# Kernel tuning notes

Measured on AMD Instinct MI355X. Metric: run time of the kernel, lower is better.

Reference implementation:

```python
import jax, jax.numpy as jnp
import numpy as np

D_MODEL = 1024
N_HEADS = 16
D_FF = 4 * D_MODEL
CTX = 2048
EPS = 1e-5


def setup_inputs() -> dict:
    key = jax.random.key(0)
    ks = jax.random.split(key, 8)
    s = 0.02
    z = jax.random.normal(ks[0], (2, CTX, D_MODEL), dtype=jnp.float32)
    W_Q = jax.random.normal(ks[1], (D_MODEL, D_MODEL), dtype=jnp.float32) * s
    W_K = jax.random.normal(ks[2], (D_MODEL, D_MODEL), dtype=jnp.float32) * s
    W_V = jax.random.normal(ks[3], (D_MODEL, D_MODEL), dtype=jnp.float32) * s
    W_O = jax.random.normal(ks[4], (D_MODEL, D_MODEL), dtype=jnp.float32) * s
    W_fc = jax.random.normal(ks[5], (D_MODEL, D_FF), dtype=jnp.float32) * s
    W_proj = jax.random.normal(ks[6], (D_FF, D_MODEL), dtype=jnp.float32) * s
    g1 = jnp.ones((D_MODEL,), dtype=jnp.float32)
    g2 = jnp.ones((D_MODEL,), dtype=jnp.float32)
    return {"z": z, "W_Q": W_Q, "W_K": W_K, "W_V": W_V, "W_O": W_O,
            "W_fc": W_fc, "W_proj": W_proj, "g1": g1, "g2": g2}


def rmsnorm(x, gain):
    rms = jnp.sqrt(jnp.sum(x * x, axis=-1, keepdims=True) / x.shape[-1] + EPS)
    return (x / rms) * gain


def gelu_erf(x):
    return x * 0.5 * (1.0 + jax.lax.erf(x / jnp.sqrt(2.0).astype(x.dtype)))


def attention(zn, W_Q, W_K, W_V, W_O):
    B, T, D = zn.shape
    H = N_HEADS
    dh = D // H
    # [B,T,D] -> [B,H,T,dh]
    def split(x):
        return x.reshape(B, T, H, dh).transpose(0, 2, 1, 3)
    Q = split(zn @ W_Q)
    K = split(zn @ W_K)
    V = split(zn @ W_V)
    scores = jnp.einsum('bhtd,bhsd->bhts', Q, K) / jnp.sqrt(jnp.float32(dh))
    causal = jnp.triu(jnp.ones((T, T), dtype=bool), k=1)  # True above diagonal -> masked
    scores = jnp.where(causal[None, None], -jnp.inf, scores)
    weights = jax.nn.softmax(scores, axis=-1)
    ctx = jnp.einsum('bhts,bhsd->bhtd', weights, V)
    ctx = ctx.transpose(0, 2, 1, 3).reshape(B, T, D)
    return ctx @ W_O


def reference(z, W_Q, W_K, W_V, W_O, W_fc, W_proj, g1, g2):
    # pre-norm GPT block: z + attn(norm1(z)); then + ffn(norm2(z))
    z = z + attention(rmsnorm(z, g1), W_Q, W_K, W_V, W_O)
    h = rmsnorm(z, g2)
    ffn = gelu_erf(h @ W_fc) @ W_proj
    return z + ffn
```

## Files before the change

kernel.cpp:

```cpp
#include <hip/hip_runtime.h>
#include <hip/hip_bf16.h>
#include <math.h>


typedef __bf16 bf16x8 __attribute__((ext_vector_type(8)));
typedef float  f32x4  __attribute__((ext_vector_type(4)));

#define MFMA_16x16x32_BF16(A, B, C) __builtin_amdgcn_mfma_f32_16x16x32_bf16((A), (B), (C), 0, 0, 0)

#define GLDS16(g, l) __builtin_amdgcn_global_load_lds( \
    (const __attribute__((address_space(1))) void*)(g), \
    (__attribute__((address_space(3))) void*)(l), 16, 0, 0)

__global__ __launch_bounds__(256) void fused_head_kernel(
    const float* __restrict__ W_Q, const float* __restrict__ W_K,
    const float* __restrict__ W_V, const float* __restrict__ W_O,
    const float* __restrict__ W_fc, const float* __restrict__ W_proj,
    __bf16* __restrict__ WtQKV, __bf16* __restrict__ WtO,
    __bf16* __restrict__ Wtfc, __bf16* __restrict__ Wtproj,
    const float* __restrict__ z, const float* __restrict__ g1,
    __bf16* __restrict__ zn)
{
    const int id = blockIdx.x;
    if (id >= 12288) {
        const int row = id - 12288, t = threadIdx.x;
        const float4 v = ((const float4*)(z + (size_t)row * 1024))[t];
        float ss = v.x * v.x + v.y * v.y + v.z * v.z + v.w * v.w;
#pragma unroll
        for (int m = 1; m < 64; m <<= 1) ss += __shfl_xor(ss, m);
        __shared__ float red[4];
        const int wid = t >> 6, lane = t & 63;
        if (lane == 0) red[wid] = ss;
        __syncthreads();
        const float tot = red[0] + red[1] + red[2] + red[3];
        const float inv = rsqrtf(tot * (1.0f / 1024.0f) + 1e-5f);
        const float4 gv = ((const float4*)g1)[t];
        __bf16* o = zn + (size_t)row * 1024 + t * 4;
        o[0] = (__bf16)(v.x * inv * gv.x);
        o[1] = (__bf16)(v.y * inv * gv.y);
        o[2] = (__bf16)(v.z * inv * gv.z);
        o[3] = (__bf16)(v.w * inv * gv.w);
        return;
    }
    const float* src;
    __bf16* dst;
    int K, N, nx, t;
    if (id < 4096) {
        const int wsel = id >> 10;
        t = id & 1023;
        src = (wsel == 0) ? W_Q : (wsel == 1) ? W_K : (wsel == 2) ? W_V : W_O;
        dst = (wsel < 3) ? (WtQKV + (size_t)wsel * 1048576) : WtO;
        K = 1024; N = 1024; nx = 32;
    } else if (id < 8192) {
        t = id - 4096; src = W_fc; dst = Wtfc; K = 1024; N = 4096; nx = 128;
    } else {
        t = id - 8192; src = W_proj; dst = Wtproj; K = 4096; N = 1024; nx = 32;
    }
    const int n0 = (t % nx) * 32, k0 = (t / nx) * 32;

    __shared__ float tile[32][33];
    const int c = threadIdx.x & 31, r = threadIdx.x >> 5;
#pragma unroll
    for (int i = 0; i < 4; ++i)
        tile[r + 8 * i][c] = src[(size_t)(k0 + r + 8 * i) * N + n0 + c];
    __syncthreads();
#pragma unroll
    for (int i = 0; i < 4; ++i)
        dst[(size_t)(n0 + r + 8 * i) * K + k0 + c] = (__bf16)tile[c][r + 8 * i];
}

__global__ __launch_bounds__(256) void rmsnorm_kernel(
    const float* __restrict__ x, const float* __restrict__ gain,
    __bf16* __restrict__ out)
{
    const int row = blockIdx.x, t = threadIdx.x;
    const float4 v = ((const float4*)(x + (size_t)row * 1024))[t];
    float ss = v.x * v.x + v.y * v.y + v.z * v.z + v.w * v.w;
#pragma unroll
    for (int m = 1; m < 64; m <<= 1) ss += __shfl_xor(ss, m);
    __shared__ float red[4];
    const int wid = t >> 6, lane = t & 63;
    if (lane == 0) red[wid] = ss;
    __syncthreads();
    const float tot = red[0] + red[1] + red[2] + red[3];
    const float inv = rsqrtf(tot * (1.0f / 1024.0f) + 1e-5f);
    const float4 gv = ((const float4*)gain)[t];
    __bf16* o = out + (size_t)row * 1024 + t * 4;
    o[0] = (__bf16)(v.x * inv * gv.x);
    o[1] = (__bf16)(v.y * inv * gv.y);
    o[2] = (__bf16)(v.z * inv * gv.z);
    o[3] = (__bf16)(v.w * inv * gv.w);
}

__global__ __launch_bounds__(256) void reduce_add_kernel(
    float* __restrict__ out, const float* __restrict__ p0,
    const float* __restrict__ p1, int n4)
{
    for (int i = blockIdx.x * 256 + threadIdx.x; i < n4; i += gridDim.x * 256) {
        const float4 a = ((const float4*)p0)[i];
        const float4 b = ((const float4*)p1)[i];
        float4 o = ((float4*)out)[i];
        o.x += a.x + b.x; o.y += a.y + b.y;
        o.z += a.z + b.z; o.w += a.w + b.w;
        ((float4*)out)[i] = o;
    }
}

template <int EPI>
__device__ __forceinline__ void epi_write(
    void* outp, const float* res, int N, int rowg, int colg, float v)
{
    if constexpr (EPI == 1) {
        const size_t idx = (size_t)rowg * N + colg;
        ((float*)outp)[idx] = res[idx] + v;
    } else if constexpr (EPI == 2) {
        const size_t idx = (size_t)rowg * N + colg;
        const float u = v * (1.0f + 0.044715f * v * v) * 2.3022585093f;
        const float r = __builtin_amdgcn_rcpf(1.0f + exp2f(u));
        ((__bf16*)outp)[idx] = (__bf16)(v - v * r);
    } else {
        __bf16* base = (__bf16*)outp;
        const int seg = colg >> 10;
        const int cg = colg & 1023;
        if (seg < 2) {
            base[(size_t)seg * 4194304 + (size_t)rowg * 1024 + cg] = (__bf16)v;
        } else {
            const int tt = rowg & 2047;
            const int r32 = tt & 31;
            const int p = ((r32 & 12) << 1) | ((r32 >> 2) & 4) | (r32 & 3);
            base[8388608 +
                 ((size_t)((rowg >> 11) * 16 + (cg >> 6)) * 64 + (cg & 63)) * 2048 +
                 ((tt & ~31) | p)] = (__bf16)v;
        }
    }
}

template <int EPI>
__global__ __launch_bounds__(512, 2) void gemm256(
    const __bf16* __restrict__ A, const __bf16* __restrict__ Bt,
    void* __restrict__ outp, const float* __restrict__ res,
    int M, int N, int K)
{
    __shared__ __bf16 As[2][2][128 * 64];
    __shared__ __bf16 Bs[2][2][128 * 64];
    const int tid = threadIdx.x;

    const int gx = gridDim.x, nwg = gx * gridDim.y;
    int bid = blockIdx.y * gx + blockIdx.x;
    int m0, n0;
    if (gx == 16 && gridDim.y == 16) {
        const int xcd = bid & 7, c = bid >> 3;
        const int rm = xcd >> 1, rn = xcd & 1;
        m0 = (rm * 4 + (c >> 3)) * 256;
        n0 = (rn * 8 + (c & 7)) * 256;
    } else {
        if ((nwg & 7) == 0) bid = (bid & 7) * (nwg >> 3) + (bid >> 3);
        m0 = (bid / gx) * 256; n0 = (bid % gx) * 256;
    }

    const int lane = tid & 63, w = tid >> 6;
    const int wr = w >> 2, wc = w & 3;
    const int lr = lane & 15, g = lane >> 4;
    const int srow8 = lane >> 3, schunk = (lane & 7) ^ srow8;
    const int xk = lr & 7;
    const int wch = wc >> 1, bro = (wc & 1) * 64;

    const __bf16* Ab = A + (size_t)m0 * K;
    const __bf16* Bb = Bt + (size_t)n0 * K;

    auto STG = [&](const __bf16* gb, __bf16* lds, int kt, int half) {
        const __bf16* src = gb + (size_t)(half * 128) * K + (kt << 6);
#pragma unroll
        for (int j = 0; j < 2; ++j) {
            const int sidx = j * 8 + w;
            GLDS16(src + (size_t)(sidx * 8 + srow8) * K + schunk * 8, lds + sidx * 512);
        }
    };

    f32x4 acc[8][4] = {};
    bf16x8 af[2][4], bf[2][4];

#define LAF(BUF, QM) do {                                                       \
    _Pragma("unroll") for (int i_ = 0; i_ < 4; ++i_)                            \
    _Pragma("unroll") for (int kk_ = 0; kk_ < 2; ++kk_)                         \
        af[kk_][i_] = *(const bf16x8*)&As[BUF][wr]                              \
            [((QM) * 64 + i_ * 16 + lr) * 64 + (((kk_ * 4 + g) ^ xk) << 3)];    \
    } while (0)

#define LBF(BUF, QN) do {                                                       \
    _Pragma("unroll") for (int i_ = 0; i_ < 2; ++i_)                            \
    _Pragma("unroll") for (int kk_ = 0; kk_ < 2; ++kk_)                         \
        bf[kk_][(QN) * 2 + i_] = *(const bf16x8*)&Bs[BUF][wch]                  \
            [(bro + ((QN) * 2 + i_) * 16 + lr) * 64 + (((kk_ * 4 + g) ^ xk) << 3)]; \
    } while (0)

#define MMQ(QM, QN) do {                                                        \
    __builtin_amdgcn_s_setprio(1);                                              \
    _Pragma("unroll") for (int kk_ = 0; kk_ < 2; ++kk_)                         \
    _Pragma("unroll") for (int i_ = 0; i_ < 4; ++i_)                            \
    _Pragma("unroll") for (int n_ = 0; n_ < 2; ++n_)                            \
        acc[(QM) * 4 + i_][(QN) * 2 + n_] = MFMA_16x16x32_BF16(                 \
            af[kk_][i_], bf[kk_][(QN) * 2 + n_], acc[(QM) * 4 + i_][(QN) * 2 + n_]); \
    __builtin_amdgcn_s_setprio(0);                                              \
    } while (0)

#define BAR()  __builtin_amdgcn_s_barrier()
#define VMC(N_) asm volatile("s_waitcnt vmcnt(" #N_ ")" ::: "memory")
#define SGB0() __builtin_amdgcn_sched_barrier(0)

    const int nt = K >> 6, niter = nt >> 1;

    STG(Ab, &As[0][0][0], 0, 0); STG(Ab, &As[0][1][0], 0, 1);
    STG(Bb, &Bs[0][0][0], 0, 0); STG(Bb, &Bs[0][1][0], 0, 1);
    STG(Bb, &Bs[1][0][0], 1, 0); STG(Bb, &Bs[1][1][0], 1, 1);

    for (int i = 0; i < niter - 1; ++i) {
        const int t1 = 2 * i + 1;
        STG(Ab, &As[1][0][0], t1, 0);
        VMC(6); BAR(); SGB0();
        LAF(0, 0); LBF(0, 0); MMQ(0, 0); BAR();
        LBF(0, 1); STG(Ab, &As[1][1][0], t1, 1); BAR(); MMQ(0, 1); BAR();
        LAF(0, 1); STG(Bb, &Bs[0][0][0], t1 + 1, 0); BAR(); MMQ(1, 0); BAR();
        STG(Bb, &Bs[0][1][0], t1 + 1, 1); BAR(); MMQ(1, 1); BAR();
        STG(Ab, &As[0][0][0], t1 + 1, 0);
        VMC(6); BAR(); SGB0();
        LAF(1, 0); LBF(1, 0); MMQ(0, 0); BAR();
        LBF(1, 1); STG(Ab, &As[0][1][0], t1 + 1, 1); BAR(); MMQ(0, 1); BAR();
        LAF(1, 1); STG(Bb, &Bs[1][0][0], t1 + 2, 0); BAR(); MMQ(1, 0); BAR();
        STG(Bb, &Bs[1][1][0], t1 + 2, 1); BAR(); MMQ(1, 1); BAR();
    }
    {
        STG(Ab, &As[1][0][0], nt - 1, 0);
        VMC(6); BAR(); SGB0();
        LAF(0, 0); LBF(0, 0); MMQ(0, 0); BAR();
        LBF(0, 1); STG(Ab, &As[1][1][0], nt - 1, 1); BAR(); MMQ(0, 1); BAR();
        LAF(0, 1); BAR(); MMQ(1, 0); BAR();
        BAR(); MMQ(1, 1); BAR();
        VMC(0); BAR(); SGB0();
        LAF(1, 0); LBF(1, 0); MMQ(0, 0); BAR();
        LBF(1, 1); BAR(); MMQ(0, 1); BAR();
        LAF(1, 1); BAR(); MMQ(1, 0); BAR();
        BAR(); MMQ(1, 1); BAR();
    }
#undef LAF
#undef LBF
#undef MMQ
#undef BAR
#undef VMC
#undef SGB0

#pragma unroll
    for (int mi = 0; mi < 8; ++mi)
#pragma unroll
        for (int ni = 0; ni < 4; ++ni) {
            const int colg = n0 + wc * 64 + ni * 16 + lr;
#pragma unroll
            for (int r = 0; r < 4; ++r) {
                const int rowg = m0 + wr * 128 + mi * 16 + 4 * g + r;
                epi_write<EPI>(outp, res, N, rowg, colg, acc[mi][ni][r]);
            }
        }
}

template <int BM, int BN, int EPI>
__global__ __launch_bounds__(256) void gemm_bf16(
    const __bf16* __restrict__ A, const __bf16* __restrict__ Bt,
    void* __restrict__ outp, const float* __restrict__ res,
    int M, int N, int K, int Kld)
{
    __shared__ __bf16 As[2][BM * 64];
    __shared__ __bf16 Bs[2][BN * 64];
    const int tid = threadIdx.x;

    const int gx = gridDim.x, nwg = gx * gridDim.y;
    int bid = blockIdx.y * gx + blockIdx.x;
    int m0, n0;
    if constexpr (EPI == 4) {
        const int xcd = bid & 7, c = bid >> 3;
        const int rm = xcd >> 1, rn = xcd & 1;
        m0 = (rm * 8 + c / 12) * BM;
        n0 = (rn * 12 + c % 12) * BN;
    } else {
        if ((nwg & 7) == 0) bid = (bid & 7) * (nwg >> 3) + (bid >> 3);
        m0 = (bid / gx) * BM; n0 = (bid % gx) * BN;
    }

    const int lane = tid & 63, w = tid >> 6;
    const int wm = w >> 1, wn = w & 1;
    const int lr = lane & 15, g = lane >> 4;
    const int srow = lane >> 3;
    const int scol = ((lane & 7) ^ srow) * 8;
    const int xr8 = lr & 7;

    constexpr int MI = BM / 32, NI = BN / 32;
    f32x4 acc[MI][NI] = {};

    const __bf16* Abase = A + (size_t)m0 * Kld + blockIdx.z * K;
    const __bf16* Bbase = Bt + (size_t)n0 * Kld + blockIdx.z * K;

    auto STAGE = [&](int kb, int buf) {
#pragma unroll
        for (int j = 0; j < BM / 32; ++j) {
            const int s = j * 4 + w;
            GLDS16(Abase + (size_t)(s * 8 + srow) * Kld + kb + scol, &As[buf][s * 512]);
        }
#pragma unroll
        for (int j = 0; j < BN / 32; ++j) {
            const int s = j * 4 + w;
            GLDS16(Bbase + (size_t)(s * 8 + srow) * Kld + kb + scol, &Bs[buf][s * 512]);
        }
    };

    const int nt = K >> 6;
    STAGE(0, 0);
    __syncthreads();

    for (int t = 0; t < nt; ++t) {
        const int cur = t & 1;
        if (t + 1 < nt) STAGE((t + 1) << 6, cur ^ 1);

        bf16x8 af[2][MI], bfr[2][NI];
#pragma unroll
        for (int kk = 0; kk < 2; ++kk) {
#pragma unroll
            for (int i = 0; i < MI; ++i)
                af[kk][i] = *(const bf16x8*)
                    &As[cur][(wm * (BM / 2) + i * 16 + lr) * 64 + (((kk * 4 + g) ^ xr8) << 3)];
#pragma unroll
            for (int i = 0; i < NI; ++i)
                bfr[kk][i] = *(const bf16x8*)
                    &Bs[cur][(wn * (BN / 2) + i * 16 + lr) * 64 + (((kk * 4 + g) ^ xr8) << 3)];
        }
#pragma unroll
        for (int kk = 0; kk < 2; ++kk)
#pragma unroll
            for (int mi = 0; mi < MI; ++mi)
#pragma unroll
                for (int ni = 0; ni < NI; ++ni)
                    acc[mi][ni] = MFMA_16x16x32_BF16(af[kk][mi], bfr[kk][ni], acc[mi][ni]);
        if (t + 1 < nt) __syncthreads();
    }

#pragma unroll
    for (int mi = 0; mi < MI; ++mi)
#pragma unroll
        for (int ni = 0; ni < NI; ++ni) {
            const int colg = n0 + wn * (BN / 2) + ni * 16 + lr;
#pragma unroll
            for (int r = 0; r < 4; ++r) {
                const int rowg = m0 + wm * (BM / 2) + mi * 16 + 4 * g + r;
                const float v = acc[mi][ni][r];
                if constexpr (EPI == 5) {
                    float* pout = (blockIdx.z == 0) ? (float*)outp : (float*)(void*)res;
                    pout[(size_t)rowg * N + colg] = v;
                } else {
                    epi_write<EPI>(outp, res, N, rowg, colg, v);
                }
            }
        }
}

__global__ __launch_bounds__(512) void attn_kernel(
    const __bf16* __restrict__ Q, const __bf16* __restrict__ Kb,
    const __bf16* __restrict__ Vt, __bf16* __restrict__ ctx)
{
    const int Dm = 1024, T = 2048;
    const int tid = threadIdx.x;
    const int w = tid >> 6, lane = tid & 63;
    const int lr = lane & 15, g = lane >> 4;
    const int bx = blockIdx.x;
    const int j = bx >> 5, bh = bx & 31, b = bh >> 4, h = bh & 15;
    const int qc = (j < 8) ? j : 23 - j;
    const int qbase = qc * 128 + w * 16;
    const size_t rowoff = (size_t)b * T;
    const __bf16* Qp = Q + rowoff * Dm + h * 64;
    const __bf16* Kp = Kb + rowoff * Dm + h * 64;
    const __bf16* Vtp = Vt + (size_t)bh * 64 * 2048;

    __shared__ __bf16 Ks[2][128 * 64];
    __shared__ __bf16 Vs[2][64 * 128];

    bf16x8 qf0 = *(const bf16x8*)&Qp[(size_t)(qbase + lr) * Dm + g * 8];
    bf16x8 qf1 = *(const bf16x8*)&Qp[(size_t)(qbase + lr) * Dm + 32 + g * 8];
    const float qsc = 0.125f * 1.44269504088896340736f;
#pragma unroll
    for (int jj = 0; jj < 8; ++jj) {
        qf0[jj] = (__bf16)((float)qf0[jj] * qsc);
        qf1[jj] = (__bf16)((float)qf1[jj] * qsc);
    }

    const int ksrow = lane >> 3;
    const int kschunk = (lane & 7) ^ ksrow;
    const int vsrow = lane >> 4;

    f32x4 acc[4] = {};
    float m_s = -__builtin_inff(), lpart = 0.0f;
    const int nsteps = qc + 1;
    const f32x4 zacc = {0.0f, 0.0f, 0.0f, 0.0f};
    const int x8 = lr & 7;
    const int qg = qbase + lr;

    auto STAGE = [&](int kvb, int buf) {
#pragma unroll
        for (int jj = 0; jj < 2; ++jj) {
            const int krow = w * 16 + jj * 8;
            GLDS16(Kp + (size_t)(kvb + krow + ksrow) * Dm + kschunk * 8,
                   &Ks[buf][krow * 64]);
            const int vrow = w * 8 + jj * 4;
            const int vchunk = (lane & 15) ^ ((vrow + vsrow) & 15);
            GLDS16(Vtp + (size_t)(vrow + vsrow) * T + kvb + vchunk * 8,
                   &Vs[buf][vrow * 128]);
        }
    };

    STAGE(0, 0);
    __syncthreads();

    for (int t = 0; t < nsteps; ++t) {
        const int kvb = t * 128, cur = t & 1;
        if (t + 1 < nsteps) STAGE(kvb + 128, cur ^ 1);

        float sv[8][4];
        if (t < qc) {
#pragma unroll
            for (int s4 = 0; s4 < 8; ++s4) {
                const int row = s4 * 16 + lr;
                const bf16x8 kfa = *(const bf16x8*)&Ks[cur][row * 64 + ((g ^ x8) << 3)];
                const bf16x8 kfb = *(const bf16x8*)&Ks[cur][row * 64 + (((4 + g) ^ x8) << 3)];
                f32x4 st = MFMA_16x16x32_BF16(kfa, qf0, zacc);
                st = MFMA_16x16x32_BF16(kfb, qf1, st);
#pragma unroll
                for (int r = 0; r < 4; ++r) sv[s4][r] = st[r];
            }
        } else {
#pragma unroll
            for (int s4 = 0; s4 < 8; ++s4) {
                const int kv0 = kvb + s4 * 16;
                if (kv0 <= qbase + 15) {
                    const int row = s4 * 16 + lr;
                    const bf16x8 kfa = *(const bf16x8*)&Ks[cur][row * 64 + ((g ^ x8) << 3)];
                    const bf16x8 kfb = *(const bf16x8*)&Ks[cur][row * 64 + (((4 + g) ^ x8) << 3)];
                    f32x4 st = MFMA_16x16x32_BF16(kfa, qf0, zacc);
                    st = MFMA_16x16x32_BF16(kfb, qf1, st);
                    const bool domask = (kv0 + 15 > qbase);
#pragma unroll
                    for (int r = 0; r < 4; ++r) {
                        float x = st[r];
                        if (domask && (kv0 + 4 * g + r > qg)) x = -__builtin_inff();
                        sv[s4][r] = x;
                    }
                } else {
#pragma unroll
                    for (int r = 0; r < 4; ++r) sv[s4][r] = -__builtin_inff();
                }
            }
        }

        float tml = sv[0][0];
#pragma unroll
        for (int s4 = 0; s4 < 8; ++s4)
#pragma unroll
            for (int r = 0; r < 4; ++r) tml = fmaxf(tml, sv[s4][r]);

        if (!__all(tml - m_s <= 11.5f)) {
            float tm = fmaxf(tml, __shfl_xor(tml, 16));
            tm = fmaxf(tm, __shfl_xor(tm, 32));
            const float m_new = fmaxf(m_s, tm);
            const float corr = exp2f(m_s - m_new);
            lpart *= corr;
            float cr[4];
#pragma unroll
            for (int r = 0; r < 4; ++r) cr[r] = __shfl(corr, 4 * g + r);
#pragma unroll
            for (int ct = 0; ct < 4; ++ct) {
                acc[ct][0] *= cr[0]; acc[ct][1] *= cr[1];
                acc[ct][2] *= cr[2]; acc[ct][3] *= cr[3];
            }
            m_s = m_new;
        }

        float rsl = 0.0f;
#pragma unroll
        for (int s4 = 0; s4 < 8; ++s4)
#pragma unroll
            for (int r = 0; r < 4; ++r) {
                sv[s4][r] = exp2f(sv[s4][r] - m_s);
                rsl += sv[s4][r];
            }
        lpart += rsl;

        bf16x8 pa[4];
#pragma unroll
        for (int s = 0; s < 4; ++s)
#pragma unroll
            for (int r = 0; r < 4; ++r) {
                pa[s][r] = (__bf16)sv[2 * s][r];
                pa[s][4 + r] = (__bf16)sv[2 * s + 1][r];
            }
        if (t < qc) {
#pragma unroll
            for (int ct = 0; ct < 4; ++ct) {
                const __bf16* vrow = &Vs[cur][(ct * 16 + lr) * 128];
#pragma unroll
                for (int s = 0; s < 4; ++s) {
                    const bf16x8 vf = *(const bf16x8*)&vrow[(((s * 4 + g) ^ lr) << 3)];
                    acc[ct] = MFMA_16x16x32_BF16(pa[s], vf, acc[ct]);
                }
            }
        } else {
#pragma unroll
            for (int ct = 0; ct < 4; ++ct) {
                const __bf16* vrow = &Vs[cur][(ct * 16 + lr) * 128];
#pragma unroll
                for (int s = 0; s < 4; ++s) {
                    if (kvb + s * 32 <= qbase + 15) {
                        const bf16x8 vf = *(const bf16x8*)&vrow[(((s * 4 + g) ^ lr) << 3)];
                        acc[ct] = MFMA_16x16x32_BF16(pa[s], vf, acc[ct]);
                    }
                }
            }
        }
        __syncthreads();
    }

    lpart += __shfl_xor(lpart, 16);
    lpart += __shfl_xor(lpart, 32);
    const float il = __builtin_amdgcn_rcpf(lpart);
    float dn[4];
#pragma unroll
    for (int r = 0; r < 4; ++r) dn[r] = __shfl(il, 4 * g + r);
#pragma unroll
    for (int ct = 0; ct < 4; ++ct)
#pragma unroll
        for (int r = 0; r < 4; ++r)
            ctx[(rowoff + qbase + 4 * g + r) * Dm + h * 64 + ct * 16 + lr] =
                (__bf16)(acc[ct][r] * dn[r]);
}

extern "C" void kernel_launch(void* const* d_in, const int* in_sizes, int n_in,
                              void* d_out, int out_size, void* d_ws, size_t ws_size,
                              hipStream_t stream)
{
    (void)in_sizes; (void)n_in; (void)out_size; (void)ws_size;
    const float* z      = (const float*)d_in[0];
    const float* W_Q    = (const float*)d_in[1];
    const float* W_K    = (const float*)d_in[2];
    const float* W_V    = (const float*)d_in[3];
    const float* W_O    = (const float*)d_in[4];
    const float* W_fc   = (const float*)d_in[5];
    const float* W_proj = (const float*)d_in[6];
    const float* g1     = (const float*)d_in[7];
    const float* g2     = (const float*)d_in[8];
    float* out = (float*)d_out;

    char* ws = (char*)d_ws;
    const size_t MB = (size_t)1 << 20;
    __bf16* WtQKV  = (__bf16*)(ws + 0 * MB);
    __bf16* WtO    = (__bf16*)(ws + 6 * MB);
    __bf16* Wtfc   = (__bf16*)(ws + 8 * MB);
    __bf16* Wtproj = (__bf16*)(ws + 16 * MB);
    __bf16* zn     = (__bf16*)(ws + 24 * MB);
    __bf16* Qb     = (__bf16*)(ws + 32 * MB);
    __bf16* Kbuf   = (__bf16*)(ws + 40 * MB);
    __bf16* Vtb    = (__bf16*)(ws + 48 * MB);
    __bf16* ffn1   = (__bf16*)(ws + 40 * MB);
    float*  part0  = (float*)(ws + 0 * MB);
    float*  part1  = (float*)(ws + 24 * MB);
    __bf16* ctx    = zn;
    __bf16* hb     = Qb;

    const int Tt = 2048, Dm = 1024, Bb = 2, M = Bb * Tt, DFF = 4096;
    const dim3 blk256(256), blk512(512);

    fused_head_kernel<<<16384, blk256, 0, stream>>>(
        W_Q, W_K, W_V, W_O, W_fc, W_proj, WtQKV, WtO, Wtfc, Wtproj, z, g1, zn);

    gemm_bf16<128, 128, 4><<<dim3(24, 32), blk256, 0, stream>>>(
        zn, WtQKV, Qb, nullptr, M, 3072, Dm, Dm);

    attn_kernel<<<512, blk512, 0, stream>>>(Qb, Kbuf, Vtb, ctx);

    gemm_bf16<128, 64, 1><<<dim3(16, 32), blk256, 0, stream>>>(
        ctx, WtO, out, z, M, Dm, Dm, Dm);

    rmsnorm_kernel<<<M, blk256, 0, stream>>>(out, g2, hb);

    gemm256<2><<<dim3(16, 16), blk512, 0, stream>>>(
        hb, Wtfc, ffn1, nullptr, M, DFF, Dm);

    gemm_bf16<128, 128, 5><<<dim3(8, 32, 2), blk256, 0, stream>>>(
        ffn1, Wtproj, part0, (const float*)part1, M, Dm, DFF / 2, DFF);

    reduce_add_kernel<<<2048, blk256, 0, stream>>>(out, part0, part1, M * Dm / 4);
}
```

Baseline: 235.0 us.

## Store split-K partials in bf16 and retile QKV GEMM to 128x96 tiles

The two split-K partial sums of the FFN down-projection are now written and read as bf16 instead of fp32, which halves the intermediate traffic in the GEMM epilogue and in the reduction kernel. The QKV projection GEMM switches from 128x128 to 128x96 tiles on a 32x32 grid, with the XCD-aware block mapping updated to match. This raises the number of workgroups, which should help fill the CUs. The cost is that rounding the partial sums to bf16 adds error to the output, and the 96-wide tile may make MFMA and shared-memory tiling less efficient.

```diff
diff --git a/kernel.cpp b/kernel.cpp
--- a/kernel.cpp
+++ b/kernel.cpp
@@ -93,16 +93,20 @@
 }
 
 __global__ __launch_bounds__(256) void reduce_add_kernel(
-    float* __restrict__ out, const float* __restrict__ p0,
-    const float* __restrict__ p1, int n4)
-{
-    for (int i = blockIdx.x * 256 + threadIdx.x; i < n4; i += gridDim.x * 256) {
-        const float4 a = ((const float4*)p0)[i];
-        const float4 b = ((const float4*)p1)[i];
-        float4 o = ((float4*)out)[i];
-        o.x += a.x + b.x; o.y += a.y + b.y;
-        o.z += a.z + b.z; o.w += a.w + b.w;
-        ((float4*)out)[i] = o;
+    float* __restrict__ out, const __bf16* __restrict__ p0,
+    const __bf16* __restrict__ p1, int n8)
+{
+    for (int i = blockIdx.x * 256 + threadIdx.x; i < n8; i += gridDim.x * 256) {
+        const bf16x8 a = ((const bf16x8*)p0)[i];
+        const bf16x8 b = ((const bf16x8*)p1)[i];
+        float4 o0 = ((float4*)out)[2 * i];
+        float4 o1 = ((float4*)out)[2 * i + 1];
+        o0.x += (float)a[0] + (float)b[0]; o0.y += (float)a[1] + (float)b[1];
+        o0.z += (float)a[2] + (float)b[2]; o0.w += (float)a[3] + (float)b[3];
+        o1.x += (float)a[4] + (float)b[4]; o1.y += (float)a[5] + (float)b[5];
+        o1.z += (float)a[6] + (float)b[6]; o1.w += (float)a[7] + (float)b[7];
+        ((float4*)out)[2 * i] = o0;
+        ((float4*)out)[2 * i + 1] = o1;
     }
 }
 
@@ -278,8 +282,8 @@
     if constexpr (EPI == 4) {
         const int xcd = bid & 7, c = bid >> 3;
         const int rm = xcd >> 1, rn = xcd & 1;
-        m0 = (rm * 8 + c / 12) * BM;
-        n0 = (rn * 12 + c % 12) * BN;
+        m0 = (rm * 8 + (c >> 4)) * BM;
+        n0 = (rn * 16 + (c & 15)) * BN;
     } else {
         if ((nwg & 7) == 0) bid = (bid & 7) * (nwg >> 3) + (bid >> 3);
         m0 = (bid / gx) * BM; n0 = (bid % gx) * BN;
@@ -351,8 +355,9 @@
                 const int rowg = m0 + wm * (BM / 2) + mi * 16 + 4 * g + r;
                 const float v = acc[mi][ni][r];
                 if constexpr (EPI == 5) {
-                    float* pout = (blockIdx.z == 0) ? (float*)outp : (float*)(void*)res;
-                    pout[(size_t)rowg * N + colg] = v;
+                    __bf16* pout = (blockIdx.z == 0) ? (__bf16*)outp
+                                                     : (__bf16*)(void*)res;
+                    pout[(size_t)rowg * N + colg] = (__bf16)v;
                 } else {
                     epi_write<EPI>(outp, res, N, rowg, colg, v);
                 }
@@ -564,8 +569,8 @@
     __bf16* Kbuf   = (__bf16*)(ws + 40 * MB);
     __bf16* Vtb    = (__bf16*)(ws + 48 * MB);
     __bf16* ffn1   = (__bf16*)(ws + 40 * MB);
-    float*  part0  = (float*)(ws + 0 * MB);
-    float*  part1  = (float*)(ws + 24 * MB);
+    __bf16* part0  = (__bf16*)(ws + 0 * MB);
+    __bf16* part1  = (__bf16*)(ws + 24 * MB);
     __bf16* ctx    = zn;
     __bf16* hb     = Qb;
 
@@ -575,7 +580,7 @@
     fused_head_kernel<<<16384, blk256, 0, stream>>>(
         W_Q, W_K, W_V, W_O, W_fc, W_proj, WtQKV, WtO, Wtfc, Wtproj, z, g1, zn);
 
-    gemm_bf16<128, 128, 4><<<dim3(24, 32), blk256, 0, stream>>>(
+    gemm_bf16<128, 96, 4><<<dim3(32, 32), blk256, 0, stream>>>(
         zn, WtQKV, Qb, nullptr, M, 3072, Dm, Dm);
 
     attn_kernel<<<512, blk512, 0, stream>>>(Qb, Kbuf, Vtb, ctx);
@@ -591,5 +596,5 @@
     gemm_bf16<128, 128, 5><<<dim3(8, 32, 2), blk256, 0, stream>>>(
         ffn1, Wtproj, part0, (const float*)part1, M, Dm, DFF / 2, DFF);
 
-    reduce_add_kernel<<<2048, blk256, 0, stream>>>(out, part0, part1, M * Dm / 4);
-}
+    reduce_add_kernel<<<2048, blk256, 0, stream>>>(out, part0, part1, M * Dm / 8);
+}
```

New measurement: 232.8 us. Within noise of the previous version (-0.9%).
